# Kernel tuning notes

Hardware: AMD Instinct MI355X
Metric: run time of the kernel (lower is better)

The kernel has to match this reference:

```python
import jax, jax.numpy as jnp
import numpy as np

B, T, C, H = 16, 2048, 1024, 64

def setup_inputs() -> dict:
    key = jax.random.key(0)
    kx, kq, kk, kv = jax.random.split(key, 4)
    x = jax.random.normal(kx, (B, T, C), dtype=jnp.float32)
    Wq = jax.random.normal(kq, (C, H), dtype=jnp.float32) * (C ** -0.5)
    Wk = jax.random.normal(kk, (C, H), dtype=jnp.float32) * (C ** -0.5)
    Wv = jax.random.normal(kv, (C, H), dtype=jnp.float32) * (C ** -0.5)
    return {"x": x, "Wq": Wq, "Wk": Wk, "Wv": Wv}

def reference(x, Wq, Wk, Wv):
    # q,k,v: [B,T,H]
    q = jnp.einsum('btc,ch->bth', x, Wq)
    k = jnp.einsum('btc,ch->bth', x, Wk)
    v = jnp.einsum('btc,ch->bth', x, Wv)
    scale = k.shape[-1] ** -0.5
    # scores: [B,T,T], causal mask then softmax (dropout=0 -> identity)
    w = jnp.einsum('bth,bsh->bts', q, k) * scale
    causal = jnp.tril(jnp.ones((x.shape[1], x.shape[1]), dtype=bool))
    w = jnp.where(causal[None, :, :], w, -jnp.inf)
    w = jax.nn.softmax(w, axis=-1)
    out = jnp.einsum('bts,bsh->bth', w, v)
    return out
```

## Files before the change

### kernel.cpp

```cpp
#include <hip/hip_runtime.h>


#define B_ 16
#define T_ 2048
#define C_ 1024
#define H_ 64
#define QK_ELEMS (B_ * T_ * H_)

typedef float  f32x4  __attribute__((ext_vector_type(4)));
typedef __bf16 bf16x8 __attribute__((ext_vector_type(8)));
typedef __bf16 bf16x4 __attribute__((ext_vector_type(4)));

__device__ __forceinline__ void glds16(const void* g, void* l) {
    __builtin_amdgcn_global_load_lds(
        (const __attribute__((address_space(1))) void*)g,
        (__attribute__((address_space(3))) void*)l, 16, 0, 0);
}

__global__ __launch_bounds__(256) void wt_kernel(const float* __restrict__ Wq,
                                                 const float* __restrict__ Wk,
                                                 const float* __restrict__ Wv,
                                                 __bf16* __restrict__ Wt) {
    __shared__ float tl[64][65];
    const int mat = blockIdx.x >> 4;
    const int c0  = (blockIdx.x & 15) * 64;
    const float* W = (mat == 0) ? Wq : (mat == 1) ? Wk : Wv;
    const int t  = threadIdx.x;
    const int r4 = t >> 6;
    const int cc = t & 63;
#pragma unroll
    for (int i = 0; i < 16; i++) {
        const int c = r4 + i * 4;
        tl[c][cc] = W[(size_t)(c0 + c) * H_ + cc];
    }
    __syncthreads();
#pragma unroll
    for (int i = 0; i < 16; i++) {
        const int h = r4 + i * 4;
        const int cc2 = ((((cc >> 3) ^ (h & 7)) << 3) | (cc & 7));
        Wt[(size_t)mat * 65536 + (size_t)h * C_ + c0 + cc2] = (__bf16)tl[cc][h];
    }
}

__global__ __launch_bounds__(256) void qkv_kernel(const float* __restrict__ x,
                                                  const __bf16* __restrict__ Wt,
                                                  __bf16* __restrict__ Qw,
                                                  __bf16* __restrict__ Kw,
                                                  __bf16* __restrict__ Vtw) {
    __shared__ __align__(16) __bf16 Blds[2][192 * 64];

    const int tid  = threadIdx.x;
    const int w    = tid >> 6;
    const int lane = tid & 63;
    const int quad = lane >> 4;
    const int l15  = lane & 15;
    const int wm   = (w & 1) * 32;
    const int wn   = (w >> 1) * 96;
    const int m0   = blockIdx.x * 64;

    f32x4 acc[12];
#pragma unroll
    for (int i = 0; i < 12; i++) acc[i] = (f32x4){0.f, 0.f, 0.f, 0.f};

    const float* xA0 = x + (size_t)(m0 + wm + l15) * C_ + quad * 8;
    const float* xA1 = xA0 + 16 * C_;

    float4 a[8];
    auto loadA = [&](int k0) {
#pragma unroll
        for (int kh = 0; kh < 2; kh++) {
            a[kh * 4 + 0] = *(const float4*)(xA0 + k0 + kh * 32);
            a[kh * 4 + 1] = *(const float4*)(xA0 + k0 + kh * 32 + 4);
            a[kh * 4 + 2] = *(const float4*)(xA1 + k0 + kh * 32);
            a[kh * 4 + 3] = *(const float4*)(xA1 + k0 + kh * 32 + 4);
        }
    };

    const __bf16* bsrc = Wt + (size_t)(w * 48 + (lane >> 3)) * C_ + (lane & 7) * 8;
    auto asyncB = [&](int k0, int buf) {
        __bf16* dst = &Blds[buf][(w * 48) * 64];
        const __bf16* src = bsrc + k0;
#pragma unroll
        for (int i = 0; i < 6; i++)
            glds16(src + (size_t)i * 8 * C_, dst + i * 8 * 64);
    };

    asyncB(0, 0);
    loadA(0);

    for (int k = 0; k < 16; k++) {
        __syncthreads();

        bf16x8 af[2][2];
#pragma unroll
        for (int kh = 0; kh < 2; kh++)
#pragma unroll
            for (int mt = 0; mt < 2; mt++) {
                const float4 p = a[kh * 4 + mt * 2 + 0];
                const float4 q = a[kh * 4 + mt * 2 + 1];
                bf16x8 v;
                v[0]=(__bf16)p.x; v[1]=(__bf16)p.y; v[2]=(__bf16)p.z; v[3]=(__bf16)p.w;
                v[4]=(__bf16)q.x; v[5]=(__bf16)q.y; v[6]=(__bf16)q.z; v[7]=(__bf16)q.w;
                af[mt][kh] = v;
            }

        const int kn = k + 1;
        if (kn < 16) { asyncB(kn * 64, kn & 1); loadA(kn * 64); }
        const int buf = k & 1;
#pragma unroll
        for (int kh = 0; kh < 2; kh++) {
            const int ch8 = ((((kh << 2) + quad) ^ (l15 & 7)) << 3);
#pragma unroll
            for (int nt = 0; nt < 6; nt++) {
                bf16x8 bfr = *(const bf16x8*)&Blds[buf][(wn + nt * 16 + l15) * 64 + ch8];
                acc[nt]     = __builtin_amdgcn_mfma_f32_16x16x32_bf16(af[0][kh], bfr, acc[nt], 0, 0, 0);
                acc[6 + nt] = __builtin_amdgcn_mfma_f32_16x16x32_bf16(af[1][kh], bfr, acc[6 + nt], 0, 0, 0);
            }
        }
    }

#pragma unroll
    for (int mt = 0; mt < 2; mt++) {
        const int row0 = m0 + wm + mt * 16 + quad * 4;
#pragma unroll
        for (int nt = 0; nt < 6; nt++) {
            const int col = wn + nt * 16 + l15;
            const f32x4 acv = acc[mt * 6 + nt];
            if (wn + nt * 16 < 64) {
#pragma unroll
                for (int r = 0; r < 4; r++)
                    Qw[(size_t)(row0 + r) * H_ + col] = (__bf16)acv[r];
            } else if (wn + nt * 16 < 128) {
                const int h = col - 64;
#pragma unroll
                for (int r = 0; r < 4; r++) {
                    const int row = row0 + r;
                    const int hs  = (((h >> 3) ^ (row & 7)) << 3) | (h & 7);
                    Kw[(size_t)row * H_ + hs] = (__bf16)acv[r];
                }
            }
        }
    }
    __syncthreads();
    __bf16* Vt_l = &Blds[0][0];
    if (w >= 2) {
#pragma unroll
        for (int mt = 0; mt < 2; mt++) {
            const int t0 = wm + mt * 16 + quad * 4;
#pragma unroll
            for (int nt = 2; nt < 6; nt++) {
                const int h = (nt - 2) * 16 + l15;
                const f32x4 acv = acc[mt * 6 + nt];
                bf16x4 pv;
                pv[0]=(__bf16)acv[0]; pv[1]=(__bf16)acv[1];
                pv[2]=(__bf16)acv[2]; pv[3]=(__bf16)acv[3];
                *(bf16x4*)&Vt_l[h * 72 + t0] = pv;
            }
        }
    }
    __syncthreads();
    if (w >= 2) {
        const int bb   = m0 >> 11;
        const int tblk = m0 & 2047;
#pragma unroll
        for (int i = 0; i < 4; i++) {
            const int hh = (w - 2) * 32 + i * 8 + (lane >> 3);
            const int cs = (((lane & 7) ^ (lane >> 3)) << 3);
            *(bf16x8*)(Vtw + (((size_t)(bb * H_ + hh)) << 11) + tblk + ((lane & 7) << 3)) =
                *(const bf16x8*)&Vt_l[hh * 72 + cs];
        }
    }
}

#define SCALE_LOG2E 0.18033688011112042f

__global__ __launch_bounds__(256) void attn_kernel(const __bf16* __restrict__ Qw,
                                                   const __bf16* __restrict__ Kw,
                                                   const __bf16* __restrict__ Vtw,
                                                   float* __restrict__ Opart,
                                                   float* __restrict__ Lpart) {
    __shared__ __align__(16) __bf16 Klds[2][64 * 64];
    __shared__ __align__(16) __bf16 Vlds[2][64 * 64];
    __shared__ __align__(16) __bf16 Plds[2][4][16 * 72];

    const int tid  = threadIdx.x;
    const int w    = tid >> 6;
    const int lane = tid & 63;
    const int quad = lane >> 4;
    const int l15  = lane & 15;

    const int b   = blockIdx.x & 15;
    const int cid = blockIdx.x >> 4;
    int i, ci;
    if (cid < 16)      { i = 15 - (cid >> 2); ci = cid & 3; }
    else if (cid < 28) { const int u = cid - 16; i = 11 - u / 3; ci = u % 3; }
    else if (cid < 36) { const int u = cid - 28; i = 7 - (u >> 1); ci = u & 1; }
    else               { i = 3 - (cid - 36); ci = 0; }

    const int jmax = 2 * i + 1;
    const int j0 = ci * 8;
    const int j1 = (j0 + 8 < jmax + 1) ? j0 + 8 : jmax + 1;
    const int nj = j1 - j0;
    const int qA0 = 2 * i * 64;
    const size_t bT = (size_t)b * T_;

    const __bf16* qpA = Qw + (bT + qA0 + w * 16 + l15) * H_ + quad * 8;
    const bf16x8 qfA0 = *(const bf16x8*)qpA;
    const bf16x8 qfA1 = *(const bf16x8*)(qpA + 32);
    const bf16x8 qfB0 = *(const bf16x8*)(qpA + 64 * H_);
    const bf16x8 qfB1 = *(const bf16x8*)(qpA + 64 * H_ + 32);

    float lA = 0.f, lB = 0.f;
    f32x4 accA[4], accB[4];
#pragma unroll
    for (int nt = 0; nt < 4; nt++) {
        accA[nt] = (f32x4){0.f, 0.f, 0.f, 0.f};
        accB[nt] = (f32x4){0.f, 0.f, 0.f, 0.f};
    }

    auto stage = [&](int ts0, int buf) {
        const __bf16* Ks = Kw + (bT + ts0) * H_;
        const __bf16* Vs = Vtw + (((size_t)(b * H_)) << 11) + ts0;
#pragma unroll
        for (int c = 0; c < 2; c++) {
            const int g   = w * 2 + c;
            const int row = g * 8 + (lane >> 3);
            const int cb  = (lane & 7) * 8;
            glds16(Ks + (size_t)row * H_ + cb, &Klds[buf][g * 512]);
            glds16(Vs + ((size_t)row << 11) + cb, &Vlds[buf][g * 512]);
        }
    };

    stage(j0 * 64, 0);

    for (int jj = 0; jj < nj; jj++) {
        const int j = j0 + jj;
        __syncthreads();
        if (jj + 1 < nj) stage((j + 1) * 64, (jj + 1) & 1);
        const int buf = jj & 1;
        const bool doA = (j <= 2 * i);
        const int ts0 = j * 64;
        const int qgA = qA0 + w * 16 + l15;

#pragma unroll
        for (int nt = 0; nt < 4; nt++) {
            const __bf16* kb = &Klds[buf][(nt * 16 + l15) * 64];
            bf16x8 kf0 = *(const bf16x8*)(kb + ((quad ^ (l15 & 7)) << 3));
            bf16x8 kf1 = *(const bf16x8*)(kb + (((4 + quad) ^ (l15 & 7)) << 3));
            const int key0 = ts0 + nt * 16 + quad * 4;

            if (doA) {
                f32x4 z = (f32x4){0.f, 0.f, 0.f, 0.f};
                z = __builtin_amdgcn_mfma_f32_16x16x32_bf16(kf0, qfA0, z, 0, 0, 0);
                z = __builtin_amdgcn_mfma_f32_16x16x32_bf16(kf1, qfA1, z, 0, 0, 0);
                bf16x4 pv;
#pragma unroll
                for (int r = 0; r < 4; r++) {
                    float e = exp2f(__builtin_fmaf(z[r], SCALE_LOG2E, -8.0f));
                    if (j == 2 * i && key0 + r > qgA) e = 0.f;
                    pv[r] = (__bf16)e;
                    lA += e;
                }
                *(bf16x4*)&Plds[0][w][l15 * 72 + nt * 16 + quad * 4] = pv;
            }
            {
                f32x4 z = (f32x4){0.f, 0.f, 0.f, 0.f};
                z = __builtin_amdgcn_mfma_f32_16x16x32_bf16(kf0, qfB0, z, 0, 0, 0);
                z = __builtin_amdgcn_mfma_f32_16x16x32_bf16(kf1, qfB1, z, 0, 0, 0);
                bf16x4 pv;
#pragma unroll
                for (int r = 0; r < 4; r++) {
                    float e = exp2f(__builtin_fmaf(z[r], SCALE_LOG2E, -8.0f));
                    if (j == jmax && key0 + r > qgA + 64) e = 0.f;
                    pv[r] = (__bf16)e;
                    lB += e;
                }
                *(bf16x4*)&Plds[1][w][l15 * 72 + nt * 16 + quad * 4] = pv;
            }
        }
        __asm__ __volatile__("s_waitcnt lgkmcnt(0)" ::: "memory");

        const __bf16* prA = &Plds[0][w][l15 * 72];
        const __bf16* prB = &Plds[1][w][l15 * 72];
        bf16x8 pfA0, pfA1;
        if (doA) {
            pfA0 = *(const bf16x8*)(prA + quad * 8);
            pfA1 = *(const bf16x8*)(prA + 32 + quad * 8);
        }
        bf16x8 pfB0 = *(const bf16x8*)(prB + quad * 8);
        bf16x8 pfB1 = *(const bf16x8*)(prB + 32 + quad * 8);
#pragma unroll
        for (int nt = 0; nt < 4; nt++) {
            const __bf16* vb = &Vlds[buf][(nt * 16 + l15) * 64];
            bf16x8 vf0 = *(const bf16x8*)(vb + ((quad ^ (l15 & 7)) << 3));
            bf16x8 vf1 = *(const bf16x8*)(vb + (((4 + quad) ^ (l15 & 7)) << 3));
            if (doA) {
                accA[nt] = __builtin_amdgcn_mfma_f32_16x16x32_bf16(pfA0, vf0, accA[nt], 0, 0, 0);
                accA[nt] = __builtin_amdgcn_mfma_f32_16x16x32_bf16(pfA1, vf1, accA[nt], 0, 0, 0);
            }
            accB[nt] = __builtin_amdgcn_mfma_f32_16x16x32_bf16(pfB0, vf0, accB[nt], 0, 0, 0);
            accB[nt] = __builtin_amdgcn_mfma_f32_16x16x32_bf16(pfB1, vf1, accB[nt], 0, 0, 0);
        }
    }

    lA += __shfl_xor(lA, 16); lA += __shfl_xor(lA, 32);
    lB += __shfl_xor(lB, 16); lB += __shfl_xor(lB, 32);

    const int qiA = 2 * i;
    const int slotA = ((((b << 5) + qiA) << 2) + ci);
    const int slotB = ((((b << 5) + qiA + 1) << 2) + ci);
    float* OpA = Opart + (size_t)slotA * 4096;
    float* OpB = Opart + (size_t)slotB * 4096;
#pragma unroll
    for (int nt = 0; nt < 4; nt++)
#pragma unroll
        for (int r = 0; r < 4; r++) {
            const int o = (w * 16 + quad * 4 + r) * 64 + nt * 16 + l15;
            OpA[o] = accA[nt][r];
            OpB[o] = accB[nt][r];
        }
    if (quad == 0) {
        Lpart[slotA * 64 + w * 16 + l15] = lA;
        Lpart[slotB * 64 + w * 16 + l15] = lB;
    }
}

__global__ __launch_bounds__(256) void reduce_kernel(const float* __restrict__ Opart,
                                                     const float* __restrict__ Lpart,
                                                     float* __restrict__ out) {
    const int b  = blockIdx.x & 15;
    const int qi = blockIdx.x >> 4;
    const int nc = ((qi & ~1) + 9) >> 3;
    const int tid = threadIdx.x;
    const int q  = tid >> 2;
    const int hc = (tid & 3) * 16;
    const int sbase = ((b << 5) + qi) << 2;

    f32x4 s[4];
#pragma unroll
    for (int i = 0; i < 4; i++) s[i] = (f32x4){0.f, 0.f, 0.f, 0.f};
    float l = 0.f;
    for (int ci = 0; ci < nc; ci++) {
        const float* Op = Opart + (size_t)(sbase + ci) * 4096 + q * 64 + hc;
#pragma unroll
        for (int i = 0; i < 4; i++) s[i] += *(const f32x4*)(Op + i * 4);
        l += Lpart[(sbase + ci) * 64 + q];
    }
    const float inv = 1.f / l;
    float* o = out + ((size_t)b * T_ + qi * 64 + q) * H_ + hc;
#pragma unroll
    for (int i = 0; i < 4; i++) {
        f32x4 r = s[i] * inv;
        *(f32x4*)(o + i * 4) = r;
    }
}

extern "C" void kernel_launch(void* const* d_in, const int* in_sizes, int n_in,
                              void* d_out, int out_size, void* d_ws, size_t ws_size,
                              hipStream_t stream) {
    const float* x  = (const float*)d_in[0];
    const float* Wq = (const float*)d_in[1];
    const float* Wk = (const float*)d_in[2];
    const float* Wv = (const float*)d_in[3];
    float* out = (float*)d_out;

    __bf16* Qw  = (__bf16*)d_ws;
    __bf16* Kw  = Qw + QK_ELEMS;
    __bf16* Vtw = Kw + QK_ELEMS;
    __bf16* Wt  = Vtw + QK_ELEMS;
    float* Opart = (float*)((char*)d_ws + 16777216);
    float* Lpart = Opart + (size_t)2048 * 4096;

    wt_kernel<<<dim3(48), dim3(256), 0, stream>>>(Wq, Wk, Wv, Wt);
    qkv_kernel<<<dim3((B_ * T_) / 64), dim3(256), 0, stream>>>(x, Wt, Qw, Kw, Vtw);
    attn_kernel<<<dim3(640), dim3(256), 0, stream>>>(Qw, Kw, Vtw, Opart, Lpart);
    reduce_kernel<<<dim3(512), dim3(256), 0, stream>>>(Opart, Lpart, out);
}
```

Baseline: 254.9 us.

## Split QKV projection grid so each block computes one of Q, K, V

The projection kernel now launches three times as many blocks, and each block computes a 64-row by 64-column tile for a single weight matrix instead of all 192 columns. This cuts per-thread accumulators and LDS use, and gives more blocks to spread across compute units. The cost is that each x tile is loaded and converted to bf16 three times. Blocks are ordered matrix-major, so the re-reads of the large fp32 activation tensor are unlikely to be served from cache.

```diff
diff --git a/kernel.cpp b/kernel.cpp
--- a/kernel.cpp
+++ b/kernel.cpp
@@ -47,41 +47,39 @@
                                                   __bf16* __restrict__ Qw,
                                                   __bf16* __restrict__ Kw,
                                                   __bf16* __restrict__ Vtw) {
-    __shared__ __align__(16) __bf16 Blds[2][192 * 64];
+    __shared__ __align__(16) __bf16 Blds[2][64 * 64];
 
     const int tid  = threadIdx.x;
     const int w    = tid >> 6;
     const int lane = tid & 63;
     const int quad = lane >> 4;
     const int l15  = lane & 15;
-    const int wm   = (w & 1) * 32;
-    const int wn   = (w >> 1) * 96;
-    const int m0   = blockIdx.x * 64;
-
-    f32x4 acc[12];
-#pragma unroll
-    for (int i = 0; i < 12; i++) acc[i] = (f32x4){0.f, 0.f, 0.f, 0.f};
-
-    const float* xA0 = x + (size_t)(m0 + wm + l15) * C_ + quad * 8;
-    const float* xA1 = xA0 + 16 * C_;
-
-    float4 a[8];
+    const int bid  = blockIdx.x;
+    const int mat  = bid >> 9;
+    const int m0   = (bid & 511) * 64;
+    const int wm   = w * 16;
+
+    f32x4 acc[4];
+#pragma unroll
+    for (int i = 0; i < 4; i++) acc[i] = (f32x4){0.f, 0.f, 0.f, 0.f};
+
+    const float* xA = x + (size_t)(m0 + wm + l15) * C_ + quad * 8;
+    float4 a[4];
     auto loadA = [&](int k0) {
 #pragma unroll
         for (int kh = 0; kh < 2; kh++) {
-            a[kh * 4 + 0] = *(const float4*)(xA0 + k0 + kh * 32);
-            a[kh * 4 + 1] = *(const float4*)(xA0 + k0 + kh * 32 + 4);
-            a[kh * 4 + 2] = *(const float4*)(xA1 + k0 + kh * 32);
-            a[kh * 4 + 3] = *(const float4*)(xA1 + k0 + kh * 32 + 4);
+            a[kh * 2 + 0] = *(const float4*)(xA + k0 + kh * 32);
+            a[kh * 2 + 1] = *(const float4*)(xA + k0 + kh * 32 + 4);
         }
     };
 
-    const __bf16* bsrc = Wt + (size_t)(w * 48 + (lane >> 3)) * C_ + (lane & 7) * 8;
+    const __bf16* bsrc = Wt + (size_t)mat * 65536
+                            + (size_t)(wm + (lane >> 3)) * C_ + (lane & 7) * 8;
     auto asyncB = [&](int k0, int buf) {
-        __bf16* dst = &Blds[buf][(w * 48) * 64];
+        __bf16* dst = &Blds[buf][wm * 64];
         const __bf16* src = bsrc + k0;
 #pragma unroll
-        for (int i = 0; i < 6; i++)
+        for (int i = 0; i < 2; i++)
             glds16(src + (size_t)i * 8 * C_, dst + i * 8 * 64);
     };
 
@@ -91,18 +89,16 @@
     for (int k = 0; k < 16; k++) {
         __syncthreads();
 
-        bf16x8 af[2][2];
-#pragma unroll
-        for (int kh = 0; kh < 2; kh++)
-#pragma unroll
-            for (int mt = 0; mt < 2; mt++) {
-                const float4 p = a[kh * 4 + mt * 2 + 0];
-                const float4 q = a[kh * 4 + mt * 2 + 1];
-                bf16x8 v;
-                v[0]=(__bf16)p.x; v[1]=(__bf16)p.y; v[2]=(__bf16)p.z; v[3]=(__bf16)p.w;
-                v[4]=(__bf16)q.x; v[5]=(__bf16)q.y; v[6]=(__bf16)q.z; v[7]=(__bf16)q.w;
-                af[mt][kh] = v;
-            }
+        bf16x8 af[2];
+#pragma unroll
+        for (int kh = 0; kh < 2; kh++) {
+            const float4 p = a[kh * 2 + 0];
+            const float4 q = a[kh * 2 + 1];
+            bf16x8 v;
+            v[0]=(__bf16)p.x; v[1]=(__bf16)p.y; v[2]=(__bf16)p.z; v[3]=(__bf16)p.w;
+            v[4]=(__bf16)q.x; v[5]=(__bf16)q.y; v[6]=(__bf16)q.z; v[7]=(__bf16)q.w;
+            af[kh] = v;
+        }
 
         const int kn = k + 1;
         if (kn < 16) { asyncB(kn * 64, kn & 1); loadA(kn * 64); }
@@ -111,60 +107,54 @@
         for (int kh = 0; kh < 2; kh++) {
             const int ch8 = ((((kh << 2) + quad) ^ (l15 & 7)) << 3);
 #pragma unroll
-            for (int nt = 0; nt < 6; nt++) {
-                bf16x8 bfr = *(const bf16x8*)&Blds[buf][(wn + nt * 16 + l15) * 64 + ch8];
-                acc[nt]     = __builtin_amdgcn_mfma_f32_16x16x32_bf16(af[0][kh], bfr, acc[nt], 0, 0, 0);
-                acc[6 + nt] = __builtin_amdgcn_mfma_f32_16x16x32_bf16(af[1][kh], bfr, acc[6 + nt], 0, 0, 0);
-            }
-        }
-    }
-
-#pragma unroll
-    for (int mt = 0; mt < 2; mt++) {
-        const int row0 = m0 + wm + mt * 16 + quad * 4;
-#pragma unroll
-        for (int nt = 0; nt < 6; nt++) {
-            const int col = wn + nt * 16 + l15;
-            const f32x4 acv = acc[mt * 6 + nt];
-            if (wn + nt * 16 < 64) {
-#pragma unroll
-                for (int r = 0; r < 4; r++)
-                    Qw[(size_t)(row0 + r) * H_ + col] = (__bf16)acv[r];
-            } else if (wn + nt * 16 < 128) {
-                const int h = col - 64;
-#pragma unroll
-                for (int r = 0; r < 4; r++) {
-                    const int row = row0 + r;
-                    const int hs  = (((h >> 3) ^ (row & 7)) << 3) | (h & 7);
-                    Kw[(size_t)row * H_ + hs] = (__bf16)acv[r];
-                }
-            }
-        }
-    }
-    __syncthreads();
-    __bf16* Vt_l = &Blds[0][0];
-    if (w >= 2) {
-#pragma unroll
-        for (int mt = 0; mt < 2; mt++) {
-            const int t0 = wm + mt * 16 + quad * 4;
-#pragma unroll
-            for (int nt = 2; nt < 6; nt++) {
-                const int h = (nt - 2) * 16 + l15;
-                const f32x4 acv = acc[mt * 6 + nt];
-                bf16x4 pv;
-                pv[0]=(__bf16)acv[0]; pv[1]=(__bf16)acv[1];
-                pv[2]=(__bf16)acv[2]; pv[3]=(__bf16)acv[3];
-                *(bf16x4*)&Vt_l[h * 72 + t0] = pv;
-            }
-        }
-    }
-    __syncthreads();
-    if (w >= 2) {
+            for (int nt = 0; nt < 4; nt++) {
+                bf16x8 bfr = *(const bf16x8*)&Blds[buf][(nt * 16 + l15) * 64 + ch8];
+                acc[nt] = __builtin_amdgcn_mfma_f32_16x16x32_bf16(af[kh], bfr, acc[nt], 0, 0, 0);
+            }
+        }
+    }
+
+    const int row0 = m0 + wm + quad * 4;
+    if (mat == 0) {
+#pragma unroll
+        for (int nt = 0; nt < 4; nt++) {
+            const int col = nt * 16 + l15;
+            const f32x4 acv = acc[nt];
+#pragma unroll
+            for (int r = 0; r < 4; r++)
+                Qw[(size_t)(row0 + r) * H_ + col] = (__bf16)acv[r];
+        }
+    } else if (mat == 1) {
+#pragma unroll
+        for (int nt = 0; nt < 4; nt++) {
+            const int h = nt * 16 + l15;
+            const f32x4 acv = acc[nt];
+#pragma unroll
+            for (int r = 0; r < 4; r++) {
+                const int row = row0 + r;
+                const int hs  = (((h >> 3) ^ (row & 7)) << 3) | (h & 7);
+                Kw[(size_t)row * H_ + hs] = (__bf16)acv[r];
+            }
+        }
+    } else {
+        __syncthreads();
+        __bf16* Vt_l = &Blds[0][0];
+        const int t0 = wm + quad * 4;
+#pragma unroll
+        for (int nt = 0; nt < 4; nt++) {
+            const int h = nt * 16 + l15;
+            const f32x4 acv = acc[nt];
+            bf16x4 pv;
+            pv[0]=(__bf16)acv[0]; pv[1]=(__bf16)acv[1];
+            pv[2]=(__bf16)acv[2]; pv[3]=(__bf16)acv[3];
+            *(bf16x4*)&Vt_l[h * 72 + t0] = pv;
+        }
+        __syncthreads();
         const int bb   = m0 >> 11;
         const int tblk = m0 & 2047;
 #pragma unroll
-        for (int i = 0; i < 4; i++) {
-            const int hh = (w - 2) * 32 + i * 8 + (lane >> 3);
+        for (int i = 0; i < 2; i++) {
+            const int hh = wm + i * 8 + (lane >> 3);
             const int cs = (((lane & 7) ^ (lane >> 3)) << 3);
             *(bf16x8*)(Vtw + (((size_t)(bb * H_ + hh)) << 11) + tblk + ((lane & 7) << 3)) =
                 *(const bf16x8*)&Vt_l[hh * 72 + cs];
@@ -372,7 +362,7 @@
     float* Lpart = Opart + (size_t)2048 * 4096;
 
     wt_kernel<<<dim3(48), dim3(256), 0, stream>>>(Wq, Wk, Wv, Wt);
-    qkv_kernel<<<dim3((B_ * T_) / 64), dim3(256), 0, stream>>>(x, Wt, Qw, Kw, Vtw);
+    qkv_kernel<<<dim3(1536), dim3(256), 0, stream>>>(x, Wt, Qw, Kw, Vtw);
     attn_kernel<<<dim3(640), dim3(256), 0, stream>>>(Qw, Kw, Vtw, Opart, Lpart);
     reduce_kernel<<<dim3(512), dim3(256), 0, stream>>>(Opart, Lpart, out);
 }
```

After: 275.2 us. 8.0% more time.

## Triple-buffer QKV projection loads with manual vmcnt waits and two-ahead prefetch

Applied to the files above, without the earlier changes.

The QKV projection kernel goes from double to triple buffering of the weight tile in LDS and keeps two register sets for the x tiles, so loads are issued two k-steps ahead. The per-step __syncthreads is replaced by an explicit s_waitcnt vmcnt(14) plus a barrier, so outstanding global loads can stay in flight across the barrier. The trailing steps re-issue redundant clamped loads of the last tile so the vmcnt count stays uniform. This raises LDS use and register pressure and depends on the exact count of vector memory ops per step being correct.

```diff
diff --git a/kernel.cpp b/kernel.cpp
--- a/kernel.cpp
+++ b/kernel.cpp
@@ -47,7 +47,7 @@
                                                   __bf16* __restrict__ Qw,
                                                   __bf16* __restrict__ Kw,
                                                   __bf16* __restrict__ Vtw) {
-    __shared__ __align__(16) __bf16 Blds[2][192 * 64];
+    __shared__ __align__(16) __bf16 Blds[3][192 * 64];
 
     const int tid  = threadIdx.x;
     const int w    = tid >> 6;
@@ -65,19 +65,19 @@
     const float* xA0 = x + (size_t)(m0 + wm + l15) * C_ + quad * 8;
     const float* xA1 = xA0 + 16 * C_;
 
-    float4 a[8];
-    auto loadA = [&](int k0) {
+    float4 a0[8], a1[8];
+    auto loadA = [&](float4 (&as)[8], int k0) {
 #pragma unroll
         for (int kh = 0; kh < 2; kh++) {
-            a[kh * 4 + 0] = *(const float4*)(xA0 + k0 + kh * 32);
-            a[kh * 4 + 1] = *(const float4*)(xA0 + k0 + kh * 32 + 4);
-            a[kh * 4 + 2] = *(const float4*)(xA1 + k0 + kh * 32);
-            a[kh * 4 + 3] = *(const float4*)(xA1 + k0 + kh * 32 + 4);
+            as[kh * 4 + 0] = *(const float4*)(xA0 + k0 + kh * 32);
+            as[kh * 4 + 1] = *(const float4*)(xA0 + k0 + kh * 32 + 4);
+            as[kh * 4 + 2] = *(const float4*)(xA1 + k0 + kh * 32);
+            as[kh * 4 + 3] = *(const float4*)(xA1 + k0 + kh * 32 + 4);
         }
     };
 
     const __bf16* bsrc = Wt + (size_t)(w * 48 + (lane >> 3)) * C_ + (lane & 7) * 8;
-    auto asyncB = [&](int k0, int buf) {
+    auto stageB = [&](int k0, int buf) {
         __bf16* dst = &Blds[buf][(w * 48) * 64];
         const __bf16* src = bsrc + k0;
 #pragma unroll
@@ -85,28 +85,27 @@
             glds16(src + (size_t)i * 8 * C_, dst + i * 8 * 64);
     };
 
-    asyncB(0, 0);
-    loadA(0);
-
-    for (int k = 0; k < 16; k++) {
-        __syncthreads();
+    auto step = [&](float4 (&as)[8], int k) {
+        __asm__ __volatile__("s_waitcnt vmcnt(14)" ::: "memory");
+        __builtin_amdgcn_s_barrier();
+        const int kn = (k + 2 <= 15) ? k + 2 : 15;
+        stageB(kn * 64, (k + 2) % 3);
 
         bf16x8 af[2][2];
 #pragma unroll
         for (int kh = 0; kh < 2; kh++)
 #pragma unroll
             for (int mt = 0; mt < 2; mt++) {
-                const float4 p = a[kh * 4 + mt * 2 + 0];
-                const float4 q = a[kh * 4 + mt * 2 + 1];
+                const float4 p = as[kh * 4 + mt * 2 + 0];
+                const float4 q = as[kh * 4 + mt * 2 + 1];
                 bf16x8 v;
                 v[0]=(__bf16)p.x; v[1]=(__bf16)p.y; v[2]=(__bf16)p.z; v[3]=(__bf16)p.w;
                 v[4]=(__bf16)q.x; v[5]=(__bf16)q.y; v[6]=(__bf16)q.z; v[7]=(__bf16)q.w;
                 af[mt][kh] = v;
             }
-
-        const int kn = k + 1;
-        if (kn < 16) { asyncB(kn * 64, kn & 1); loadA(kn * 64); }
-        const int buf = k & 1;
+        loadA(as, kn * 64);
+
+        const int buf = k % 3;
 #pragma unroll
         for (int kh = 0; kh < 2; kh++) {
             const int ch8 = ((((kh << 2) + quad) ^ (l15 & 7)) << 3);
@@ -117,7 +116,18 @@
                 acc[6 + nt] = __builtin_amdgcn_mfma_f32_16x16x32_bf16(af[1][kh], bfr, acc[6 + nt], 0, 0, 0);
             }
         }
-    }
+    };
+
+    stageB(0, 0);  loadA(a0, 0);
+    stageB(64, 1); loadA(a1, 64);
+
+    for (int k = 0; k < 16; k += 2) {
+        step(a0, k);
+        step(a1, k + 1);
+    }
+
+    __asm__ __volatile__("s_waitcnt vmcnt(0)" ::: "memory");
+    __syncthreads();
 
 #pragma unroll
     for (int mt = 0; mt < 2; mt++) {
@@ -141,7 +151,6 @@
             }
         }
     }
-    __syncthreads();
     __bf16* Vt_l = &Blds[0][0];
     if (w >= 2) {
 #pragma unroll
```

Measured after the change: 285.4 us. 1.12x slower.
